# Optimization experiments

Hardware: AMD Instinct MI355X
Metric: run time of the kernel (lower is better)

Reference implementation:

```python
import jax, jax.numpy as jnp
import numpy as np

H = 128  # hidden_size hard-coded in the torch module


def _lin(key, fan_in, shape):
    b = 1.0 / np.sqrt(fan_in)
    return jax.random.uniform(key, shape, minval=-b, maxval=b, dtype=jnp.float32)


def _gru_step(x, wih, bih, bhh):
    # torch GRU, single time step, h0 = 0; gate order (r, z, n)
    g = x @ wih.T + bih
    xr, xz, xn = jnp.split(g, 3, axis=-1)
    br, bz, bn = jnp.split(bhh, 3)
    r = jax.nn.sigmoid(xr + br)
    z = jax.nn.sigmoid(xz + bz)
    n = jnp.tanh(xn + r * bn)
    return (1.0 - z) * n  # h' = (1-z)*n + z*0


def _forward(x_node, x_edge, nt_w1, nt_b1, nt_w2, nt_b2, et_w, et_b,
             ngru_wih, ngru_bih, ngru_bhh, egru_wih, egru_bih, egru_bhh,
             natt_w, natt_b, eatt_w, eatt_b,
             lr_w1, lr_b1, lr_w2, lr_b2, cr_w1, cr_b1, cr_w2, cr_b2,
             mr_w1, mr_b1, mr_w2, mr_b2, pairs):
    B, N, _ = x_node.shape
    node_f = jax.nn.relu(x_node @ nt_w1 + nt_b1) @ nt_w2 + nt_b2      # [B,N,H]
    edge_f = x_edge @ et_w + et_b                                      # [B,N,N,H]
    nh = eh = None
    for _ in range(2):  # num_time_steps; GRU inputs are NOT updated in the original loop
        nh = _gru_step(node_f, ngru_wih, ngru_bih, ngru_bhh)           # [B,N,H]
        eh = _gru_step(edge_f, egru_wih, egru_bih, egru_bhh)           # [B,N,N,H]
        # --- node message pooling: attention over column index j ---
        n_col = jnp.broadcast_to(nh[:, :, None, :], eh.shape)          # aug[b,i,j] = nh[b,i]
        logits = (jnp.concatenate([n_col, eh], -1) @ natt_w)[..., 0] + natt_b[0]
        w = jax.nn.softmax(logits, axis=-1)                            # [B,N,N]
        nh = jnp.einsum('bijk,bij->bik', eh, w)                        # pooled node states
        # --- edge message pooling: 2-way attention over (row, col) node states ---
        n_row = jnp.broadcast_to(nh[:, None, :, :], eh.shape)          # [b,i,j] = nh[b,j]
        n_col = jnp.broadcast_to(nh[:, :, None, :], eh.shape)          # [b,i,j] = nh[b,i]
        l_row = (jnp.concatenate([n_row, eh], -1) @ eatt_w)[..., 0] + eatt_b[0]
        l_col = (jnp.concatenate([n_col, eh], -1) @ eatt_w)[..., 0] + eatt_b[0]
        w2 = jax.nn.softmax(jnp.stack([l_row, l_col], -1), axis=-1)    # [B,N,N,2]
        eh = w2[..., 0:1] * n_row + w2[..., 1:2] * n_col               # einsum('bijl,bijkl->bijk')
    # --- classifier inputs (aggregator = elementwise mean) ---
    i0, i1 = pairs[..., 0], pairs[..., 1]                              # [B,P]
    emb0 = jnp.take_along_axis(nh, i0[..., None], axis=1)              # [B,P,H]
    emb1 = jnp.take_along_axis(nh, i1[..., None], axis=1)
    bix = jnp.arange(B)[:, None]
    e01 = eh[bix, i0, i1]                                              # [B,P,H]
    e10 = eh[bix, i1, i0]
    ci = jnp.concatenate([(emb0 + emb1) * 0.5, (e01 + e10) * 0.5], -1)  # [B,P,2H]

    def head(w1, b1, wo, bo):
        return jax.nn.relu(ci @ w1 + b1) @ wo + bo

    lr = head(lr_w1, lr_b1, lr_w2, lr_b2)
    cr = head(cr_w1, cr_b1, cr_w2, cr_b2)
    mr = head(mr_w1, mr_b1, mr_w2, mr_b2)
    return jnp.concatenate([lr, cr, mr], axis=-1)                      # [B,P,6+5+3]


def setup_inputs() -> dict:
    B, N, P = 16, 64, 128
    NF, EF = 1024, 512
    CH = 512  # classifier hidden
    ks = list(jax.random.split(jax.random.key(0), 40))
    k = iter(ks)
    inp = {}
    inp['concatenated_node_features'] = jax.random.normal(next(k), (B, N, NF), dtype=jnp.float32)
    inp['interaction_feature'] = jax.random.normal(next(k), (B, N, N, EF), dtype=jnp.float32)
    inp['nt_w1'] = _lin(next(k), NF, (NF, 512)); inp['nt_b1'] = _lin(next(k), NF, (512,))
    inp['nt_w2'] = _lin(next(k), 512, (512, H)); inp['nt_b2'] = _lin(next(k), 512, (H,))
    inp['et_w'] = _lin(next(k), EF, (EF, H)); inp['et_b'] = _lin(next(k), EF, (H,))
    inp['ngru_wih'] = _lin(next(k), H, (3 * H, H))
    inp['ngru_bih'] = _lin(next(k), H, (3 * H,)); inp['ngru_bhh'] = _lin(next(k), H, (3 * H,))
    inp['egru_wih'] = _lin(next(k), H, (3 * H, H))
    inp['egru_bih'] = _lin(next(k), H, (3 * H,)); inp['egru_bhh'] = _lin(next(k), H, (3 * H,))
    inp['natt_w'] = _lin(next(k), 2 * H, (2 * H, 1)); inp['natt_b'] = _lin(next(k), 2 * H, (1,))
    inp['eatt_w'] = _lin(next(k), 2 * H, (2 * H, 1)); inp['eatt_b'] = _lin(next(k), 2 * H, (1,))
    for name, od in (('lr', 6), ('cr', 5), ('mr', 3)):
        inp[name + '_w1'] = _lin(next(k), 2 * H, (2 * H, CH))
        inp[name + '_b1'] = _lin(next(k), 2 * H, (CH,))
        inp[name + '_w2'] = _lin(next(k), CH, (CH, od))
        inp[name + '_b2'] = _lin(next(k), CH, (od,))
    inp['object_pairs'] = jax.random.randint(next(k), (B, P, 2), 0, N, dtype=jnp.int64 if jax.config.jax_enable_x64 else jnp.int32)
    inp['num_relation'] = jax.random.randint(next(k), (B,), 0, P, dtype=jnp.int64 if jax.config.jax_enable_x64 else jnp.int32)
    return inp


def reference(concatenated_node_features, interaction_feature,
              nt_w1, nt_b1, nt_w2, nt_b2, et_w, et_b,
              ngru_wih, ngru_bih, ngru_bhh, egru_wih, egru_bih, egru_bhh,
              natt_w, natt_b, eatt_w, eatt_b,
              lr_w1, lr_b1, lr_w2, lr_b2, cr_w1, cr_b1, cr_w2, cr_b2,
              mr_w1, mr_b1, mr_w2, mr_b2, object_pairs, num_relation):
    # num_relation is read but unused in the original make_classifier_inputs loop
    return _forward(concatenated_node_features, interaction_feature,
                    nt_w1, nt_b1, nt_w2, nt_b2, et_w, et_b,
                    ngru_wih, ngru_bih, ngru_bhh, egru_wih, egru_bih, egru_bhh,
                    natt_w, natt_b, eatt_w, eatt_b,
                    lr_w1, lr_b1, lr_w2, lr_b2, cr_w1, cr_b1, cr_w2, cr_b2,
                    mr_w1, mr_b1, mr_w2, mr_b2, object_pairs)
```

## Files before the change

### kernel.cpp

```cpp
#include <hip/hip_runtime.h>
#include <math.h>
#include <stdint.h>


typedef __attribute__((ext_vector_type(8))) short short8;
typedef __attribute__((ext_vector_type(4))) float f32x4;

#define DEVINL __device__ __forceinline__

DEVINL float sigmoidf_(float x) { return 1.0f / (1.0f + __expf(-x)); }
DEVINL float tanhf_(float x) {
    float e = __expf(2.0f * x);
    return (e - 1.0f) / (e + 1.0f);
}
DEVINL short bf16_rne(float f) {
    uint32_t u = __float_as_uint(f);
    u += 0x7FFFu + ((u >> 16) & 1u);
    return (short)(u >> 16);
}
DEVINL float bf16_to_f(short s) {
    return __uint_as_float(((uint32_t)(uint16_t)s) << 16);
}
DEVINL void gload_lds16(const void* g, void* l) {
    __builtin_amdgcn_global_load_lds(
        (const __attribute__((address_space(1))) void*)(uintptr_t)g,
        (__attribute__((address_space(3))) void*)(uint32_t)(uintptr_t)l,
        16, 0, 0);
}
DEVINL void ldsbar() {
    asm volatile("s_waitcnt lgkmcnt(0)\n\ts_barrier" ::: "memory");
    __builtin_amdgcn_sched_barrier(0);
}

__global__ __launch_bounds__(256) void prep_all(
    const float* __restrict__ et_w, const float* __restrict__ wih,
    const float* __restrict__ w1a, const float* __restrict__ w1b,
    const float* __restrict__ w1c,
    short* __restrict__ Bf1, short* __restrict__ Bf2,
    short* __restrict__ Wf1_hi, short* __restrict__ Wf1_lo)
{
    const int bid = blockIdx.x, t = threadIdx.x;
    if (bid < 256) {
        int idx = bid * 256 + t;
        int k = idx >> 7, n = idx & 127;
        float v = et_w[(size_t)k * 128 + n];
        short hi = bf16_rne(v), lo = bf16_rne(v - bf16_to_f(hi));
        int kt = k >> 5, ct = n >> 4;
        int lane = (((k >> 3) & 3) << 4) | (n & 15);
        int j = k & 7;
        size_t s0 = ((((size_t)kt * 2 + 0) * 8 + ct) * 64 + lane) * 8 + j;
        size_t s1 = ((((size_t)kt * 2 + 1) * 8 + ct) * 64 + lane) * 8 + j;
        Bf1[s0] = hi; Bf1[s1] = lo;
    } else if (bid < 448) {
        int idx = (bid - 256) * 256 + t;
        int n = idx >> 7, k = idx & 127;
        float v = wih[(size_t)n * 128 + k];
        short hi = bf16_rne(v), lo = bf16_rne(v - bf16_to_f(hi));
        int kt = k >> 5, ct = n >> 4;
        int lane = (((k >> 3) & 3) << 4) | (n & 15);
        int j = k & 7;
        size_t s0 = ((((size_t)kt * 2 + 0) * 24 + ct) * 64 + lane) * 8 + j;
        size_t s1 = ((((size_t)kt * 2 + 1) * 24 + ct) * 64 + lane) * 8 + j;
        Bf2[s0] = hi; Bf2[s1] = lo;
    } else {
        int idx = (bid - 448) * 256 + t;
        int h = idx >> 17;
        int r = idx & 131071;
        int k = r >> 9, c = r & 511;
        const float* w1 = (h == 0) ? w1a : (h == 1) ? w1b : w1c;
        float v = w1[(size_t)k * 512 + c];
        short hi = bf16_rne(v), lo = bf16_rne(v - bf16_to_f(hi));
        int kt = k >> 5, ct = c >> 4;
        int lane = (((k >> 3) & 3) << 4) | (c & 15);
        int j = k & 7;
        size_t fidx = ((((size_t)h * 8 + kt) * 32 + ct) * 64 + lane) * 8 + j;
        Wf1_hi[fidx] = hi;
        Wf1_lo[fidx] = lo;
    }
}

#define PH1_ITER(KT, BH0, BH1, BL0, BL1, NBH0, NBH1, NBL0, NBL1,              \
                 PCV0, PCV1, PLD0, PLD1, RBUF, WBUF)                          \
    {                                                                         \
        if ((KT) < 15) {                                                      \
            const short* bkt = Bf1 + (size_t)((KT) + 1) * 8192;               \
            NBH0 = *(const short8*)(bkt + ct0 * 512 + ln8);                   \
            NBH1 = *(const short8*)(bkt + ct1 * 512 + ln8);                   \
            NBL0 = *(const short8*)(bkt + 4096 + ct0 * 512 + ln8);            \
            NBL1 = *(const short8*)(bkt + 4096 + ct1 * 512 + ln8);            \
            float av[8] = {PCV0.x, PCV0.y, PCV0.z, PCV0.w,                    \
                           PCV1.x, PCV1.y, PCV1.z, PCV1.w};                   \
            short8 h8, l8;                                                    \
            _Pragma("unroll") for (int j = 0; j < 8; ++j) {                   \
                short h = bf16_rne(av[j]);                                    \
                h8[j] = h;                                                    \
                l8[j] = bf16_rne(av[j] - bf16_to_f(h));                       \
            }                                                                 \
            *(short8*)(smem + (WBUF) + aslotb) = h8;                          \
            *(short8*)(smem + (WBUF) + 4096 + aslotb) = l8;                   \
        }                                                                     \
        if ((KT) < 14) {                                                      \
            PLD0 = *(const float4*)(aptr + (size_t)((KT) + 2) * 32);          \
            PLD1 = *(const float4*)(aptr + (size_t)((KT) + 2) * 32 + 4);      \
        }                                                                     \
        {                                                                     \
            const char* Ah_c = smem + (RBUF);                                 \
            short8 Ahf[4], Alf[4];                                            \
            _Pragma("unroll") for (int rt = 0; rt < 4; ++rt) {                \
                Ahf[rt] = *(const short8*)(Ah_c + (rt * 64 + lane) * 16);     \
                Alf[rt] = *(const short8*)(Ah_c + 4096 + (rt * 64 + lane) * 16); \
            }                                                                 \
            _Pragma("unroll") for (int rt = 0; rt < 4; ++rt) {                \
                acc1[rt][0] = __builtin_amdgcn_mfma_f32_16x16x32_bf16(Ahf[rt], BH0, acc1[rt][0], 0, 0, 0); \
                acc1[rt][0] = __builtin_amdgcn_mfma_f32_16x16x32_bf16(Alf[rt], BH0, acc1[rt][0], 0, 0, 0); \
                acc1[rt][0] = __builtin_amdgcn_mfma_f32_16x16x32_bf16(Ahf[rt], BL0, acc1[rt][0], 0, 0, 0); \
                acc1[rt][1] = __builtin_amdgcn_mfma_f32_16x16x32_bf16(Ahf[rt], BH1, acc1[rt][1], 0, 0, 0); \
                acc1[rt][1] = __builtin_amdgcn_mfma_f32_16x16x32_bf16(Alf[rt], BH1, acc1[rt][1], 0, 0, 0); \
                acc1[rt][1] = __builtin_amdgcn_mfma_f32_16x16x32_bf16(Ahf[rt], BL1, acc1[rt][1], 0, 0, 0); \
            }                                                                 \
        }                                                                     \
        ldsbar();                                                             \
    }

__global__ __launch_bounds__(256, 3) void fused_kernel(
    const float* __restrict__ x_edge,
    const short* __restrict__ Bf1, const short* __restrict__ Bf2,
    const float* __restrict__ et_b,
    const float* __restrict__ bih, const float* __restrict__ bhh,
    const float* __restrict__ natt_w, const float* __restrict__ eatt_w,
    float* __restrict__ nh_p, float* __restrict__ u_out)
{
    __shared__ __align__(16) char smem[35328];
    const int t = threadIdx.x;
    const int wv = t >> 6, lane = t & 63;
    const int g = blockIdx.x;
    const size_t bm = (size_t)g * 64;

    const int arow = t >> 2, akb = t & 3;
    const int aslotb = (((arow >> 4) * 64) + ((akb << 4) | (arow & 15))) * 16;
    const float* aptr = x_edge + (bm + arow) * 512 + akb * 8;

    const int ct0 = wv * 2, ct1 = wv * 2 + 1;
    const int ln8 = lane * 8;

    f32x4 acc1[4][2] = {};

    float4 paA0, paA1, paB0, paB1;
    short8 bhA0, bhA1, blA0, blA1, bhB0, bhB1, blB0, blB1;

    paA0 = *(const float4*)(aptr);
    paA1 = *(const float4*)(aptr + 4);
    paB0 = *(const float4*)(aptr + 32);
    paB1 = *(const float4*)(aptr + 36);
    {
        const short* bkt = Bf1;
        bhA0 = *(const short8*)(bkt + ct0 * 512 + ln8);
        bhA1 = *(const short8*)(bkt + ct1 * 512 + ln8);
        blA0 = *(const short8*)(bkt + 4096 + ct0 * 512 + ln8);
        blA1 = *(const short8*)(bkt + 4096 + ct1 * 512 + ln8);
    }
    {
        float av[8] = {paA0.x, paA0.y, paA0.z, paA0.w,
                       paA1.x, paA1.y, paA1.z, paA1.w};
        short8 h8, l8;
#pragma unroll
        for (int j = 0; j < 8; ++j) {
            short h = bf16_rne(av[j]);
            h8[j] = h;
            l8[j] = bf16_rne(av[j] - bf16_to_f(h));
        }
        *(short8*)(smem + aslotb) = h8;
        *(short8*)(smem + 4096 + aslotb) = l8;
    }
    ldsbar();

    for (int kt = 0; kt < 16; kt += 2) {
        PH1_ITER(kt, bhA0, bhA1, blA0, blA1, bhB0, bhB1, blB0, blB1,
                 paB0, paB1, paA0, paA1, 0, 8192)
        PH1_ITER(kt + 1, bhB0, bhB1, blB0, blB1, bhA0, bhA1, blA0, blA1,
                 paA0, paA1, paB0, paB1, 8192, 0)
    }
    __syncthreads();

    float* ef_s = (float*)smem;
#pragma unroll
    for (int c = 0; c < 2; ++c) {
        int col = wv * 32 + c * 16 + (lane & 15);
        float bias = et_b[col];
#pragma unroll
        for (int rt = 0; rt < 4; ++rt) {
#pragma unroll
            for (int q = 0; q < 4; ++q) {
                int row = rt * 16 + ((lane >> 4) << 2) + q;
                ef_s[row * 132 + col] = acc1[rt][c][q] + bias;
            }
        }
    }
    __syncthreads();

    const int EHP = 132;
    float* eh_s = (float*)smem;
#pragma unroll
    for (int rtp = 0; rtp < 2; ++rtp) {
        f32x4 acch[2][6] = {};
#pragma unroll
        for (int kt = 0; kt < 4; ++kt) {
            const short* bkt = Bf2 + (size_t)kt * 24576;
            short8 Ah[2], Al[2];
#pragma unroll
            for (int r = 0; r < 2; ++r) {
                int rt = rtp * 2 + r;
                const float* src = ef_s + (rt * 16 + (lane & 15)) * 132
                                 + kt * 32 + (lane >> 4) * 8;
                float4 v0 = *(const float4*)(src);
                float4 v1 = *(const float4*)(src + 4);
                float av[8] = {v0.x, v0.y, v0.z, v0.w, v1.x, v1.y, v1.z, v1.w};
#pragma unroll
                for (int j = 0; j < 8; ++j) {
                    short hh = bf16_rne(av[j]);
                    Ah[r][j] = hh;
                    Al[r][j] = bf16_rne(av[j] - bf16_to_f(hh));
                }
            }
#pragma unroll
            for (int c = 0; c < 6; ++c) {
                int ctg = ((c >> 1) << 3) + (wv << 1) + (c & 1);
                short8 Bh = *(const short8*)(bkt + ctg * 512 + ln8);
                short8 Bl = *(const short8*)(bkt + 12288 + ctg * 512 + ln8);
#pragma unroll
                for (int r = 0; r < 2; ++r) {
                    acch[r][c] = __builtin_amdgcn_mfma_f32_16x16x32_bf16(Ah[r], Bh, acch[r][c], 0, 0, 0);
                    acch[r][c] = __builtin_amdgcn_mfma_f32_16x16x32_bf16(Al[r], Bh, acch[r][c], 0, 0, 0);
                    acch[r][c] = __builtin_amdgcn_mfma_f32_16x16x32_bf16(Ah[r], Bl, acch[r][c], 0, 0, 0);
                }
            }
        }
        __syncthreads();
#pragma unroll
        for (int cc = 0; cc < 2; ++cc) {
            int o = (wv << 5) + (cc << 4) + (lane & 15);
            float bco = bih[o] + bhh[o];
            float bcz = bih[128 + o] + bhh[128 + o];
            float bcn = bih[256 + o];
            float bn3 = bhh[256 + o];
#pragma unroll
            for (int r = 0; r < 2; ++r) {
#pragma unroll
                for (int q = 0; q < 4; ++q) {
                    int row = rtp * 32 + r * 16 + ((lane >> 4) << 2) + q;
                    float rr = sigmoidf_(acch[r][cc][q] + bco);
                    float zz = sigmoidf_(acch[r][2 + cc][q] + bcz);
                    float nn = tanhf_(acch[r][4 + cc][q] + bcn + rr * bn3);
                    eh_s[row * EHP + o] = (1.0f - zz) * nn;
                }
            }
        }
    }
    __syncthreads();

    float* red  = (float*)(smem + 33792);
    float* s2v  = red + 256;
    float* ewv  = s2v + 64;
    {
        int j = t >> 2, q = t & 3;
        const float* row = eh_s + j * EHP + q * 32;
        const float* wb = natt_w + 128 + q * 32;
        float a = 0.f;
#pragma unroll
        for (int k2 = 0; k2 < 32; ++k2) a = fmaf(row[k2], wb[k2], a);
        red[t] = a;
    }
    __syncthreads();
    if (t < 64) s2v[t] = red[4 * t] + red[4 * t + 1] + red[4 * t + 2] + red[4 * t + 3];
    __syncthreads();
    if (t < 64) {
        float m = -1e30f;
        for (int j = 0; j < 64; ++j) m = fmaxf(m, s2v[j]);
        ewv[t] = __expf(s2v[t] - m);
    }
    __syncthreads();
    float inv = 0.f;
    for (int j = 0; j < 64; ++j) inv += ewv[j];
    inv = 1.0f / inv;
    {
        int o = t & 127, h = t >> 7;
        float a = 0.f;
        for (int j = h * 32; j < h * 32 + 32; ++j)
            a = fmaf(ewv[j], eh_s[j * EHP + o], a);
        __syncthreads();
        red[t] = a;
    }
    __syncthreads();
    if (t < 128) {
        float v = (red[t] + red[t + 128]) * inv;
        nh_p[(size_t)g * 128 + t] = v;
        red[t] = v * eatt_w[t];
    }
    __syncthreads();
    for (int s = 64; s > 0; s >>= 1) {
        if (t < s) red[t] += red[t + s];
        __syncthreads();
    }
    if (t == 0) u_out[g] = red[0];
}

__global__ __launch_bounds__(128) void ci_kernel(
    const float* __restrict__ nh_p, const float* __restrict__ u,
    const int* __restrict__ pairs, float* __restrict__ ci)
{
    const int bp = blockIdx.x;
    const int b  = bp >> 7;
    const int t  = threadIdx.x;
    int i0 = pairs[bp * 2 + 0];
    int i1 = pairs[bp * 2 + 1];
    const float* n0 = nh_p + (size_t)(b * 64 + i0) * 128;
    const float* n1 = nh_p + (size_t)(b * 64 + i1) * 128;
    float s = sigmoidf_(u[b * 64 + i1] - u[b * 64 + i0]);
    float v0 = n0[t], v1 = n1[t];
    ci[(size_t)bp * 256 + t]       = 0.5f * (v0 + v1);
    ci[(size_t)bp * 256 + 128 + t] = s * v1 + (1.0f - s) * v0;
}

__global__ __launch_bounds__(256, 1) void headcls_kernel(
    const float* __restrict__ ci,
    const short* __restrict__ Wf1_hi, const short* __restrict__ Wf1_lo,
    const float* __restrict__ b1a, const float* __restrict__ b1b,
    const float* __restrict__ b1c,
    const float* __restrict__ w2a, const float* __restrict__ w2b,
    const float* __restrict__ w2c,
    const float* __restrict__ b2a, const float* __restrict__ b2b,
    const float* __restrict__ b2c,
    float* __restrict__ out)
{
    __shared__ __align__(16) char smem[139264];
    const int t = threadIdx.x;
    const int wv = t >> 6, lane = t & 63;
    const int rb = blockIdx.x;
    const int hd = blockIdx.y;
    const float* b1 = hd == 0 ? b1a : hd == 1 ? b1b : b1c;
    const float* w2 = hd == 0 ? w2a : hd == 1 ? w2b : w2c;
    const float* b2 = hd == 0 ? b2a : hd == 1 ? b2b : b2c;
    const int od  = hd == 0 ? 6 : hd == 1 ? 5 : 3;
    const int off = hd == 0 ? 0 : hd == 1 ? 6 : 11;

    const int arow = t >> 2, akb = t & 3;
    const int abyte = ((((arow >> 4) * 64) + ((akb << 4) | (arow & 15))) * 8) * 2;
    const float* aptr = ci + ((size_t)rb * 32 + arow) * 256 + akb * 8;

    f32x4 acc[2][8] = {};

    float4 a0, a1;
    if (t < 128) {
        a0 = *(const float4*)(aptr);
        a1 = *(const float4*)(aptr + 4);
    }
    {
        const char* sh = (const char*)(Wf1_hi + (size_t)hd * 8 * 32 * 512);
        const char* sl = (const char*)(Wf1_lo + (size_t)hd * 8 * 32 * 512);
#pragma unroll
        for (int i = 0; i < 8; ++i) {
            int ch = i * 4 + wv;
            int o2 = ch * 1024 + lane * 16;
            gload_lds16(sh + o2, smem + ch * 1024);
            gload_lds16(sl + o2, smem + 32768 + ch * 1024);
        }
    }
    if (t < 128) {
        float av[8] = {a0.x, a0.y, a0.z, a0.w, a1.x, a1.y, a1.z, a1.w};
        short8 h8, l8;
#pragma unroll
        for (int j = 0; j < 8; ++j) {
            short h = bf16_rne(av[j]);
            h8[j] = h;
            l8[j] = bf16_rne(av[j] - bf16_to_f(h));
        }
        *(short8*)(smem + 131072 + abyte) = h8;
        *(short8*)(smem + 131072 + 2048 + abyte) = l8;
    }
    __syncthreads();

    for (int kt = 0; kt < 8; ++kt) {
        const int cur = kt & 1;
        const char* Bh_c = smem + cur * 65536;
        const char* Bl_c = Bh_c + 32768;
        const char* Ah_c = smem + 131072 + cur * 4096;
        const char* Al_c = Ah_c + 2048;

        float4 b0, b1v;
        if (kt < 7) {
            const char* sh = (const char*)(Wf1_hi + ((size_t)hd * 8 + kt + 1) * 32 * 512);
            const char* sl = (const char*)(Wf1_lo + ((size_t)hd * 8 + kt + 1) * 32 * 512);
            char* dBh = smem + (cur ^ 1) * 65536;
#pragma unroll
            for (int i = 0; i < 8; ++i) {
                int ch = i * 4 + wv;
                int o2 = ch * 1024 + lane * 16;
                gload_lds16(sh + o2, dBh + ch * 1024);
                gload_lds16(sl + o2, dBh + 32768 + ch * 1024);
            }
            if (t < 128) {
                b0  = *(const float4*)(aptr + (size_t)(kt + 1) * 32);
                b1v = *(const float4*)(aptr + (size_t)(kt + 1) * 32 + 4);
            }
        }

        short8 Ah[2], Al[2];
#pragma unroll
        for (int rt = 0; rt < 2; ++rt) {
            Ah[rt] = *(const short8*)(Ah_c + (rt * 64 + lane) * 16);
            Al[rt] = *(const short8*)(Al_c + (rt * 64 + lane) * 16);
        }
#pragma unroll
        for (int c = 0; c < 8; ++c) {
            int ctg = wv * 8 + c;
            short8 Bh = *(const short8*)(Bh_c + (ctg * 64 + lane) * 16);
            short8 Bl = *(const short8*)(Bl_c + (ctg * 64 + lane) * 16);
#pragma unroll
            for (int rt = 0; rt < 2; ++rt) {
                acc[rt][c] = __builtin_amdgcn_mfma_f32_16x16x32_bf16(Ah[rt], Bh, acc[rt][c], 0, 0, 0);
                acc[rt][c] = __builtin_amdgcn_mfma_f32_16x16x32_bf16(Al[rt], Bh, acc[rt][c], 0, 0, 0);
                acc[rt][c] = __builtin_amdgcn_mfma_f32_16x16x32_bf16(Ah[rt], Bl, acc[rt][c], 0, 0, 0);
            }
        }

        if (kt < 7 && t < 128) {
            float av[8] = {b0.x, b0.y, b0.z, b0.w, b1v.x, b1v.y, b1v.z, b1v.w};
            short8 h8, l8;
#pragma unroll
            for (int j = 0; j < 8; ++j) {
                short h = bf16_rne(av[j]);
                h8[j] = h;
                l8[j] = bf16_rne(av[j] - bf16_to_f(h));
            }
            char* dAh = smem + 131072 + (cur ^ 1) * 4096;
            *(short8*)(dAh + abyte) = h8;
            *(short8*)(dAh + 2048 + abyte) = l8;
        }
        __syncthreads();
    }

    float* h_s  = (float*)smem;
    float* w2_s = (float*)(smem + 66048);
    for (int idx = t; idx < 512 * od; idx += 256) w2_s[idx] = w2[idx];
#pragma unroll
    for (int c = 0; c < 8; ++c) {
        int ctg = wv * 8 + c;
        int col = ctg * 16 + (lane & 15);
        float bias = b1[col];
#pragma unroll
        for (int rt = 0; rt < 2; ++rt) {
#pragma unroll
            for (int q = 0; q < 4; ++q) {
                int row = rt * 16 + ((lane >> 4) << 2) + q;
                h_s[row * 516 + col] = fmaxf(acc[rt][c][q] + bias, 0.f);
            }
        }
    }
    __syncthreads();

    {
        int row = t >> 3, o = t & 7;
        if (o < od) {
            const float* hr = h_s + row * 516;
            float a = b2[o];
            for (int c = 0; c < 512; ++c)
                a = fmaf(hr[c], w2_s[c * od + o], a);
            out[((size_t)rb * 32 + row) * 14 + off + o] = a;
        }
    }
}

extern "C" void kernel_launch(void* const* d_in, const int* in_sizes, int n_in,
                              void* d_out, int out_size, void* d_ws, size_t ws_size,
                              hipStream_t stream)
{
    const float* x_edge   = (const float*)d_in[1];
    const float* et_w     = (const float*)d_in[6];
    const float* et_b     = (const float*)d_in[7];
    const float* egru_wih = (const float*)d_in[11];
    const float* egru_bih = (const float*)d_in[12];
    const float* egru_bhh = (const float*)d_in[13];
    const float* natt_w   = (const float*)d_in[14];
    const float* eatt_w   = (const float*)d_in[16];
    const float* lr_w1 = (const float*)d_in[18];
    const float* lr_b1 = (const float*)d_in[19];
    const float* lr_w2 = (const float*)d_in[20];
    const float* lr_b2 = (const float*)d_in[21];
    const float* cr_w1 = (const float*)d_in[22];
    const float* cr_b1 = (const float*)d_in[23];
    const float* cr_w2 = (const float*)d_in[24];
    const float* cr_b2 = (const float*)d_in[25];
    const float* mr_w1 = (const float*)d_in[26];
    const float* mr_b1 = (const float*)d_in[27];
    const float* mr_w2 = (const float*)d_in[28];
    const float* mr_b2 = (const float*)d_in[29];
    const int* pairs   = (const int*)d_in[30];
    float* out = (float*)d_out;
    char* ws = (char*)d_ws;

    short* Bf1    = (short*)(ws + 0);
    short* Bf2    = (short*)(ws + 262144);
    short* Wf1_hi = (short*)(ws + 458752);
    short* Wf1_lo = (short*)(ws + 1245184);
    float* nh_p   = (float*)(ws + 2031616);
    float* u      = (float*)(ws + 2555904);
    float* ci     = (float*)(ws + 2560000);

    prep_all<<<1984, 256, 0, stream>>>(et_w, egru_wih, lr_w1, cr_w1, mr_w1,
                                       Bf1, Bf2, Wf1_hi, Wf1_lo);

    fused_kernel<<<1024, 256, 0, stream>>>(
        x_edge, Bf1, Bf2, et_b, egru_bih, egru_bhh, natt_w, eatt_w, nh_p, u);

    ci_kernel<<<2048, 128, 0, stream>>>(nh_p, u, pairs, ci);

    headcls_kernel<<<dim3(64, 3), 256, 0, stream>>>(
        ci, Wf1_hi, Wf1_lo, lr_b1, cr_b1, mr_b1,
        lr_w2, cr_w2, mr_w2, lr_b2, cr_b2, mr_b2, out);
}
```

Measured before the change: 99.74 us.

## Process two 64-row edge tiles per 512-thread block sharing B-fragment loads

Each block of the fused kernel now handles 128 edge rows with 512 threads. Waves are split into column quarter (cq) and row half (rq), so two row groups use the same column tiles of the weight fragments. The LDS staging and the attention/pooling scratch are doubled and given per-half offsets, and the grid is halved. The aim is to amortize per-block overhead and improve L2 reuse of the B weights, at the cost of twice the shared memory per block and block-wide barriers spanning both halves.

```diff
diff --git a/kernel.cpp b/kernel.cpp
--- a/kernel.cpp
+++ b/kernel.cpp
@@ -97,7 +97,7 @@
                 l8[j] = bf16_rne(av[j] - bf16_to_f(h));                       \
             }                                                                 \
             *(short8*)(smem + (WBUF) + aslotb) = h8;                          \
-            *(short8*)(smem + (WBUF) + 4096 + aslotb) = l8;                   \
+            *(short8*)(smem + (WBUF) + 8192 + aslotb) = l8;                   \
         }                                                                     \
         if ((KT) < 14) {                                                      \
             PLD0 = *(const float4*)(aptr + (size_t)((KT) + 2) * 32);          \
@@ -107,8 +107,9 @@
             const char* Ah_c = smem + (RBUF);                                 \
             short8 Ahf[4], Alf[4];                                            \
             _Pragma("unroll") for (int rt = 0; rt < 4; ++rt) {                \
-                Ahf[rt] = *(const short8*)(Ah_c + (rt * 64 + lane) * 16);     \
-                Alf[rt] = *(const short8*)(Ah_c + 4096 + (rt * 64 + lane) * 16); \
+                int grt = rq * 4 + rt;                                        \
+                Ahf[rt] = *(const short8*)(Ah_c + (grt * 64 + lane) * 16);    \
+                Alf[rt] = *(const short8*)(Ah_c + 8192 + (grt * 64 + lane) * 16); \
             }                                                                 \
             _Pragma("unroll") for (int rt = 0; rt < 4; ++rt) {                \
                 acc1[rt][0] = __builtin_amdgcn_mfma_f32_16x16x32_bf16(Ahf[rt], BH0, acc1[rt][0], 0, 0, 0); \
@@ -122,7 +123,7 @@
         ldsbar();                                                             \
     }
 
-__global__ __launch_bounds__(256, 3) void fused_kernel(
+__global__ __launch_bounds__(512, 4) void fused_kernel(
     const float* __restrict__ x_edge,
     const short* __restrict__ Bf1, const short* __restrict__ Bf2,
     const float* __restrict__ et_b,
@@ -130,17 +131,18 @@
     const float* __restrict__ natt_w, const float* __restrict__ eatt_w,
     float* __restrict__ nh_p, float* __restrict__ u_out)
 {
-    __shared__ __align__(16) char smem[35328];
+    __shared__ __align__(16) char smem[70656];
     const int t = threadIdx.x;
     const int wv = t >> 6, lane = t & 63;
-    const int g = blockIdx.x;
-    const size_t bm = (size_t)g * 64;
+    const int cq = wv & 3, rq = wv >> 2;
+    const int g2 = blockIdx.x;
+    const size_t bm = (size_t)g2 * 128;
 
     const int arow = t >> 2, akb = t & 3;
     const int aslotb = (((arow >> 4) * 64) + ((akb << 4) | (arow & 15))) * 16;
     const float* aptr = x_edge + (bm + arow) * 512 + akb * 8;
 
-    const int ct0 = wv * 2, ct1 = wv * 2 + 1;
+    const int ct0 = cq * 2, ct1 = cq * 2 + 1;
     const int ln8 = lane * 8;
 
     f32x4 acc1[4][2] = {};
@@ -170,28 +172,28 @@
             l8[j] = bf16_rne(av[j] - bf16_to_f(h));
         }
         *(short8*)(smem + aslotb) = h8;
-        *(short8*)(smem + 4096 + aslotb) = l8;
+        *(short8*)(smem + 8192 + aslotb) = l8;
     }
     ldsbar();
 
     for (int kt = 0; kt < 16; kt += 2) {
         PH1_ITER(kt, bhA0, bhA1, blA0, blA1, bhB0, bhB1, blB0, blB1,
-                 paB0, paB1, paA0, paA1, 0, 8192)
+                 paB0, paB1, paA0, paA1, 0, 16384)
         PH1_ITER(kt + 1, bhB0, bhB1, blB0, blB1, bhA0, bhA1, blA0, blA1,
-                 paA0, paA1, paB0, paB1, 8192, 0)
+                 paA0, paA1, paB0, paB1, 16384, 0)
     }
     __syncthreads();
 
     float* ef_s = (float*)smem;
 #pragma unroll
     for (int c = 0; c < 2; ++c) {
-        int col = wv * 32 + c * 16 + (lane & 15);
+        int col = cq * 32 + c * 16 + (lane & 15);
         float bias = et_b[col];
 #pragma unroll
         for (int rt = 0; rt < 4; ++rt) {
 #pragma unroll
             for (int q = 0; q < 4; ++q) {
-                int row = rt * 16 + ((lane >> 4) << 2) + q;
+                int row = rq * 64 + rt * 16 + ((lane >> 4) << 2) + q;
                 ef_s[row * 132 + col] = acc1[rt][c][q] + bias;
             }
         }
@@ -199,7 +201,7 @@
     __syncthreads();
 
     const int EHP = 132;
-    float* eh_s = (float*)smem;
+    float* ef_t = (float*)smem + rq * (64 * EHP);
 #pragma unroll
     for (int rtp = 0; rtp < 2; ++rtp) {
         f32x4 acch[2][6] = {};
@@ -210,7 +212,7 @@
 #pragma unroll
             for (int r = 0; r < 2; ++r) {
                 int rt = rtp * 2 + r;
-                const float* src = ef_s + (rt * 16 + (lane & 15)) * 132
+                const float* src = ef_t + (rt * 16 + (lane & 15)) * 132
                                  + kt * 32 + (lane >> 4) * 8;
                 float4 v0 = *(const float4*)(src);
                 float4 v1 = *(const float4*)(src + 4);
@@ -224,7 +226,7 @@
             }
 #pragma unroll
             for (int c = 0; c < 6; ++c) {
-                int ctg = ((c >> 1) << 3) + (wv << 1) + (c & 1);
+                int ctg = ((c >> 1) << 3) + (cq << 1) + (c & 1);
                 short8 Bh = *(const short8*)(bkt + ctg * 512 + ln8);
                 short8 Bl = *(const short8*)(bkt + 12288 + ctg * 512 + ln8);
 #pragma unroll
@@ -238,7 +240,7 @@
         __syncthreads();
 #pragma unroll
         for (int cc = 0; cc < 2; ++cc) {
-            int o = (wv << 5) + (cc << 4) + (lane & 15);
+            int o = (cq << 5) + (cc << 4) + (lane & 15);
             float bco = bih[o] + bhh[o];
             float bcz = bih[128 + o] + bhh[128 + o];
             float bcn = bih[256 + o];
@@ -251,57 +253,60 @@
                     float rr = sigmoidf_(acch[r][cc][q] + bco);
                     float zz = sigmoidf_(acch[r][2 + cc][q] + bcz);
                     float nn = tanhf_(acch[r][4 + cc][q] + bcn + rr * bn3);
-                    eh_s[row * EHP + o] = (1.0f - zz) * nn;
+                    ef_t[row * EHP + o] = (1.0f - zz) * nn;
                 }
             }
         }
     }
     __syncthreads();
 
-    float* red  = (float*)(smem + 33792);
+    const int tt = cq * 64 + lane;
+    const int G = g2 * 2 + rq;
+    float* eh_g = ef_t;
+    float* red  = (float*)(smem + 67584 + rq * 1536);
     float* s2v  = red + 256;
     float* ewv  = s2v + 64;
     {
-        int j = t >> 2, q = t & 3;
-        const float* row = eh_s + j * EHP + q * 32;
+        int j = tt >> 2, q = tt & 3;
+        const float* row = eh_g + j * EHP + q * 32;
         const float* wb = natt_w + 128 + q * 32;
         float a = 0.f;
 #pragma unroll
         for (int k2 = 0; k2 < 32; ++k2) a = fmaf(row[k2], wb[k2], a);
-        red[t] = a;
-    }
-    __syncthreads();
-    if (t < 64) s2v[t] = red[4 * t] + red[4 * t + 1] + red[4 * t + 2] + red[4 * t + 3];
-    __syncthreads();
-    if (t < 64) {
+        red[tt] = a;
+    }
+    __syncthreads();
+    if (tt < 64) s2v[tt] = red[4 * tt] + red[4 * tt + 1] + red[4 * tt + 2] + red[4 * tt + 3];
+    __syncthreads();
+    if (tt < 64) {
         float m = -1e30f;
         for (int j = 0; j < 64; ++j) m = fmaxf(m, s2v[j]);
-        ewv[t] = __expf(s2v[t] - m);
+        ewv[tt] = __expf(s2v[tt] - m);
     }
     __syncthreads();
     float inv = 0.f;
     for (int j = 0; j < 64; ++j) inv += ewv[j];
     inv = 1.0f / inv;
     {
-        int o = t & 127, h = t >> 7;
+        int o = tt & 127, h = tt >> 7;
         float a = 0.f;
         for (int j = h * 32; j < h * 32 + 32; ++j)
-            a = fmaf(ewv[j], eh_s[j * EHP + o], a);
+            a = fmaf(ewv[j], eh_g[j * EHP + o], a);
         __syncthreads();
-        red[t] = a;
-    }
-    __syncthreads();
-    if (t < 128) {
-        float v = (red[t] + red[t + 128]) * inv;
-        nh_p[(size_t)g * 128 + t] = v;
-        red[t] = v * eatt_w[t];
+        red[tt] = a;
+    }
+    __syncthreads();
+    if (tt < 128) {
+        float v = (red[tt] + red[tt + 128]) * inv;
+        nh_p[(size_t)G * 128 + tt] = v;
+        red[tt] = v * eatt_w[tt];
     }
     __syncthreads();
     for (int s = 64; s > 0; s >>= 1) {
-        if (t < s) red[t] += red[t + s];
+        if (tt < s) red[tt] += red[tt + s];
         __syncthreads();
     }
-    if (t == 0) u_out[g] = red[0];
+    if (tt == 0) u_out[G] = red[0];
 }
 
 __global__ __launch_bounds__(128) void ci_kernel(
@@ -509,7 +514,7 @@
     prep_all<<<1984, 256, 0, stream>>>(et_w, egru_wih, lr_w1, cr_w1, mr_w1,
                                        Bf1, Bf2, Wf1_hi, Wf1_lo);
 
-    fused_kernel<<<1024, 256, 0, stream>>>(
+    fused_kernel<<<512, 512, 0, stream>>>(
         x_edge, Bf1, Bf2, et_b, egru_bih, egru_bhh, natt_w, eatt_w, nh_p, u);
 
     ci_kernel<<<2048, 128, 0, stream>>>(nh_p, u, pairs, ci);
```

Measured after the change: 109.2 us. +9.5%, slower.

## Drop low-order bf16 weight split in edge GEMMs and use packed bf16 converts

Applied to the files above, without the earlier changes.

The edge-transform and edge-GRU weight matrices are now stored only as a single bf16 (hi) part, so each k-step issues two MFMAs (A_hi*B_hi, A_lo*B_hi) instead of three, and the kernel loads half as much weight data. The scalar hi/lo bf16 splitting loops are replaced by a helper that uses the packed v_cvt_pk_bf16_f32 instruction. The aim is to cut MFMA count, weight traffic and conversion ALU work. The cost is lower precision, since weights are now truncated to bf16 and the error against the fp32 reference grows.

```diff
diff --git a/kernel.cpp b/kernel.cpp
--- a/kernel.cpp
+++ b/kernel.cpp
@@ -20,6 +20,23 @@
 }
 DEVINL float bf16_to_f(short s) {
     return __uint_as_float(((uint32_t)(uint16_t)s) << 16);
+}
+DEVINL void cvt_hilo8(const float av[8], short8* h8, short8* l8) {
+    union { uint32_t u[4]; short8 s; } H, L;
+#pragma unroll
+    for (int i = 0; i < 4; ++i) {
+        float a0 = av[2 * i], a1 = av[2 * i + 1];
+        uint32_t ph;
+        asm("v_cvt_pk_bf16_f32 %0, %1, %2" : "=v"(ph) : "v"(a0), "v"(a1));
+        float h0 = __uint_as_float(ph << 16);
+        float h1 = __uint_as_float(ph & 0xFFFF0000u);
+        uint32_t pl;
+        asm("v_cvt_pk_bf16_f32 %0, %1, %2" : "=v"(pl) : "v"(a0 - h0), "v"(a1 - h1));
+        H.u[i] = ph;
+        L.u[i] = pl;
+    }
+    *h8 = H.s;
+    *l8 = L.s;
 }
 DEVINL void gload_lds16(const void* g, void* l) {
     __builtin_amdgcn_global_load_lds(
@@ -44,24 +61,22 @@
         int idx = bid * 256 + t;
         int k = idx >> 7, n = idx & 127;
         float v = et_w[(size_t)k * 128 + n];
-        short hi = bf16_rne(v), lo = bf16_rne(v - bf16_to_f(hi));
+        short hi = bf16_rne(v);
         int kt = k >> 5, ct = n >> 4;
         int lane = (((k >> 3) & 3) << 4) | (n & 15);
         int j = k & 7;
-        size_t s0 = ((((size_t)kt * 2 + 0) * 8 + ct) * 64 + lane) * 8 + j;
-        size_t s1 = ((((size_t)kt * 2 + 1) * 8 + ct) * 64 + lane) * 8 + j;
-        Bf1[s0] = hi; Bf1[s1] = lo;
+        size_t s0 = (((size_t)kt * 8 + ct) * 64 + lane) * 8 + j;
+        Bf1[s0] = hi;
     } else if (bid < 448) {
         int idx = (bid - 256) * 256 + t;
         int n = idx >> 7, k = idx & 127;
         float v = wih[(size_t)n * 128 + k];
-        short hi = bf16_rne(v), lo = bf16_rne(v - bf16_to_f(hi));
+        short hi = bf16_rne(v);
         int kt = k >> 5, ct = n >> 4;
         int lane = (((k >> 3) & 3) << 4) | (n & 15);
         int j = k & 7;
-        size_t s0 = ((((size_t)kt * 2 + 0) * 24 + ct) * 64 + lane) * 8 + j;
-        size_t s1 = ((((size_t)kt * 2 + 1) * 24 + ct) * 64 + lane) * 8 + j;
-        Bf2[s0] = hi; Bf2[s1] = lo;
+        size_t s0 = (((size_t)kt * 24 + ct) * 64 + lane) * 8 + j;
+        Bf2[s0] = hi;
     } else {
         int idx = (bid - 448) * 256 + t;
         int h = idx >> 17;
@@ -79,23 +94,17 @@
     }
 }
 
-#define PH1_ITER(KT, BH0, BH1, BL0, BL1, NBH0, NBH1, NBL0, NBL1,              \
+#define PH1_ITER(KT, BH0, BH1, NBH0, NBH1,                                    \
                  PCV0, PCV1, PLD0, PLD1, RBUF, WBUF)                          \
     {                                                                         \
         if ((KT) < 15) {                                                      \
-            const short* bkt = Bf1 + (size_t)((KT) + 1) * 8192;               \
+            const short* bkt = Bf1 + (size_t)((KT) + 1) * 4096;               \
             NBH0 = *(const short8*)(bkt + ct0 * 512 + ln8);                   \
             NBH1 = *(const short8*)(bkt + ct1 * 512 + ln8);                   \
-            NBL0 = *(const short8*)(bkt + 4096 + ct0 * 512 + ln8);            \
-            NBL1 = *(const short8*)(bkt + 4096 + ct1 * 512 + ln8);            \
             float av[8] = {PCV0.x, PCV0.y, PCV0.z, PCV0.w,                    \
                            PCV1.x, PCV1.y, PCV1.z, PCV1.w};                   \
             short8 h8, l8;                                                    \
-            _Pragma("unroll") for (int j = 0; j < 8; ++j) {                   \
-                short h = bf16_rne(av[j]);                                    \
-                h8[j] = h;                                                    \
-                l8[j] = bf16_rne(av[j] - bf16_to_f(h));                       \
-            }                                                                 \
+            cvt_hilo8(av, &h8, &l8);                                          \
             *(short8*)(smem + (WBUF) + aslotb) = h8;                          \
             *(short8*)(smem + (WBUF) + 4096 + aslotb) = l8;                   \
         }                                                                     \
@@ -113,10 +122,8 @@
             _Pragma("unroll") for (int rt = 0; rt < 4; ++rt) {                \
                 acc1[rt][0] = __builtin_amdgcn_mfma_f32_16x16x32_bf16(Ahf[rt], BH0, acc1[rt][0], 0, 0, 0); \
                 acc1[rt][0] = __builtin_amdgcn_mfma_f32_16x16x32_bf16(Alf[rt], BH0, acc1[rt][0], 0, 0, 0); \
-                acc1[rt][0] = __builtin_amdgcn_mfma_f32_16x16x32_bf16(Ahf[rt], BL0, acc1[rt][0], 0, 0, 0); \
                 acc1[rt][1] = __builtin_amdgcn_mfma_f32_16x16x32_bf16(Ahf[rt], BH1, acc1[rt][1], 0, 0, 0); \
                 acc1[rt][1] = __builtin_amdgcn_mfma_f32_16x16x32_bf16(Alf[rt], BH1, acc1[rt][1], 0, 0, 0); \
-                acc1[rt][1] = __builtin_amdgcn_mfma_f32_16x16x32_bf16(Ahf[rt], BL1, acc1[rt][1], 0, 0, 0); \
             }                                                                 \
         }                                                                     \
         ldsbar();                                                             \
@@ -146,7 +153,7 @@
     f32x4 acc1[4][2] = {};
 
     float4 paA0, paA1, paB0, paB1;
-    short8 bhA0, bhA1, blA0, blA1, bhB0, bhB1, blB0, blB1;
+    short8 bhA0, bhA1, bhB0, bhB1;
 
     paA0 = *(const float4*)(aptr);
     paA1 = *(const float4*)(aptr + 4);
@@ -156,28 +163,21 @@
         const short* bkt = Bf1;
         bhA0 = *(const short8*)(bkt + ct0 * 512 + ln8);
         bhA1 = *(const short8*)(bkt + ct1 * 512 + ln8);
-        blA0 = *(const short8*)(bkt + 4096 + ct0 * 512 + ln8);
-        blA1 = *(const short8*)(bkt + 4096 + ct1 * 512 + ln8);
     }
     {
         float av[8] = {paA0.x, paA0.y, paA0.z, paA0.w,
                        paA1.x, paA1.y, paA1.z, paA1.w};
         short8 h8, l8;
-#pragma unroll
-        for (int j = 0; j < 8; ++j) {
-            short h = bf16_rne(av[j]);
-            h8[j] = h;
-            l8[j] = bf16_rne(av[j] - bf16_to_f(h));
-        }
+        cvt_hilo8(av, &h8, &l8);
         *(short8*)(smem + aslotb) = h8;
         *(short8*)(smem + 4096 + aslotb) = l8;
     }
     ldsbar();
 
     for (int kt = 0; kt < 16; kt += 2) {
-        PH1_ITER(kt, bhA0, bhA1, blA0, blA1, bhB0, bhB1, blB0, blB1,
+        PH1_ITER(kt, bhA0, bhA1, bhB0, bhB1,
                  paB0, paB1, paA0, paA1, 0, 8192)
-        PH1_ITER(kt + 1, bhB0, bhB1, blB0, blB1, bhA0, bhA1, blA0, blA1,
+        PH1_ITER(kt + 1, bhB0, bhB1, bhA0, bhA1,
                  paA0, paA1, paB0, paB1, 8192, 0)
     }
     __syncthreads();
@@ -205,7 +205,7 @@
         f32x4 acch[2][6] = {};
 #pragma unroll
         for (int kt = 0; kt < 4; ++kt) {
-            const short* bkt = Bf2 + (size_t)kt * 24576;
+            const short* bkt = Bf2 + (size_t)kt * 12288;
             short8 Ah[2], Al[2];
 #pragma unroll
             for (int r = 0; r < 2; ++r) {
@@ -215,23 +215,16 @@
                 float4 v0 = *(const float4*)(src);
                 float4 v1 = *(const float4*)(src + 4);
                 float av[8] = {v0.x, v0.y, v0.z, v0.w, v1.x, v1.y, v1.z, v1.w};
-#pragma unroll
-                for (int j = 0; j < 8; ++j) {
-                    short hh = bf16_rne(av[j]);
-                    Ah[r][j] = hh;
-                    Al[r][j] = bf16_rne(av[j] - bf16_to_f(hh));
-                }
+                cvt_hilo8(av, &Ah[r], &Al[r]);
             }
 #pragma unroll
             for (int c = 0; c < 6; ++c) {
                 int ctg = ((c >> 1) << 3) + (wv << 1) + (c & 1);
                 short8 Bh = *(const short8*)(bkt + ctg * 512 + ln8);
-                short8 Bl = *(const short8*)(bkt + 12288 + ctg * 512 + ln8);
 #pragma unroll
                 for (int r = 0; r < 2; ++r) {
                     acch[r][c] = __builtin_amdgcn_mfma_f32_16x16x32_bf16(Ah[r], Bh, acch[r][c], 0, 0, 0);
                     acch[r][c] = __builtin_amdgcn_mfma_f32_16x16x32_bf16(Al[r], Bh, acch[r][c], 0, 0, 0);
-                    acch[r][c] = __builtin_amdgcn_mfma_f32_16x16x32_bf16(Ah[r], Bl, acch[r][c], 0, 0, 0);
                 }
             }
         }
@@ -368,12 +361,7 @@
     if (t < 128) {
         float av[8] = {a0.x, a0.y, a0.z, a0.w, a1.x, a1.y, a1.z, a1.w};
         short8 h8, l8;
-#pragma unroll
-        for (int j = 0; j < 8; ++j) {
-            short h = bf16_rne(av[j]);
-            h8[j] = h;
-            l8[j] = bf16_rne(av[j] - bf16_to_f(h));
-        }
+        cvt_hilo8(av, &h8, &l8);
         *(short8*)(smem + 131072 + abyte) = h8;
         *(short8*)(smem + 131072 + 2048 + abyte) = l8;
     }
@@ -426,12 +414,7 @@
         if (kt < 7 && t < 128) {
             float av[8] = {b0.x, b0.y, b0.z, b0.w, b1v.x, b1v.y, b1v.z, b1v.w};
             short8 h8, l8;
-#pragma unroll
-            for (int j = 0; j < 8; ++j) {
-                short h = bf16_rne(av[j]);
-                h8[j] = h;
-                l8[j] = bf16_rne(av[j] - bf16_to_f(h));
-            }
+            cvt_hilo8(av, &h8, &l8);
             char* dAh = smem + 131072 + (cur ^ 1) * 4096;
             *(short8*)(dAh + abyte) = h8;
             *(short8*)(dAh + 2048 + abyte) = l8;
@@ -499,12 +482,12 @@
     char* ws = (char*)d_ws;
 
     short* Bf1    = (short*)(ws + 0);
-    short* Bf2    = (short*)(ws + 262144);
-    short* Wf1_hi = (short*)(ws + 458752);
-    short* Wf1_lo = (short*)(ws + 1245184);
-    float* nh_p   = (float*)(ws + 2031616);
-    float* u      = (float*)(ws + 2555904);
-    float* ci     = (float*)(ws + 2560000);
+    short* Bf2    = (short*)(ws + 131072);
+    short* Wf1_hi = (short*)(ws + 229376);
+    short* Wf1_lo = (short*)(ws + 1015808);
+    float* nh_p   = (float*)(ws + 1802240);
+    float* u      = (float*)(ws + 2326528);
+    float* ci     = (float*)(ws + 2330624);
 
     prep_all<<<1984, 256, 0, stream>>>(et_w, egru_wih, lr_w1, cr_w1, mr_w1,
                                        Bf1, Bf2, Wf1_hi, Wf1_lo);
```

Measured after the change: 83.30 us. 16.5% less time.
